# Performance work log

Hardware: AMD Instinct MI355X
Metric: run time of the kernel (lower is better)

## Reference

```python
import jax, jax.numpy as jnp
import numpy as np

V, E, H = 50000, 200, 128
B, R, S, W = 16, 10, 20, 64


def gru_last(x, lengths, Wih, Whh, bih, bhh, reverse=False):
    # x: [N,T,D], lengths: [N] -> final valid hidden state [N,H]
    # Masked-update scan: h only updates on valid timesteps, so after the full
    # scan h equals the packed-sequence final hidden (fwd: t=len-1; bwd: t=0).
    N, T, _ = x.shape
    Hd = Whh.shape[1]
    xi = x @ Wih.T + bih                      # [N,T,3H] input gates, precomputed
    t = jnp.arange(T)
    if reverse:
        xi = xi[:, ::-1]
        valid = (T - 1 - t)[None, :] < lengths[:, None]
    else:
        valid = t[None, :] < lengths[:, None]

    def step(h, inp):
        xg, v = inp
        hg = h @ Whh.T + bhh
        r = jax.nn.sigmoid(xg[:, :Hd] + hg[:, :Hd])
        z = jax.nn.sigmoid(xg[:, Hd:2 * Hd] + hg[:, Hd:2 * Hd])
        n = jnp.tanh(xg[:, 2 * Hd:] + r * hg[:, 2 * Hd:])
        hn = (1.0 - z) * n + z * h
        return jnp.where(v[:, None], hn, h), None

    h0 = jnp.zeros((N, Hd), x.dtype)
    hT, _ = jax.lax.scan(step, h0, (jnp.swapaxes(xi, 0, 1), valid.T))
    return hT


def bigru_last(x, lengths, pf, pb):
    hf = gru_last(x, lengths, *pf, reverse=False)
    hb = gru_last(x, lengths, *pb, reverse=True)
    return 0.5 * (hf + hb)  # reduce bidirectional h_n to hid_dim (mean of dirs)


def setup_inputs() -> dict:
    key = jax.random.key(0)
    ks = jax.random.split(key, 24)

    def gn(k, shape, s=0.1):
        return jax.random.normal(k, shape, dtype=jnp.float32) * s

    return {
        "inputs": jax.random.randint(ks[0], (B, R, S, W), 0, V),
        "sent_lengths": jax.random.randint(ks[1], (B, R, S), 1, W + 1),
        "sent_counts": jax.random.randint(ks[2], (B, R), 1, S + 1),
        "embed": gn(ks[3], (V, E), 1.0),
        "wWih_f": gn(ks[4], (3 * H, E)), "wWhh_f": gn(ks[5], (3 * H, H)),
        "wbih_f": gn(ks[6], (3 * H,)), "wbhh_f": gn(ks[7], (3 * H,)),
        "wWih_b": gn(ks[8], (3 * H, E)), "wWhh_b": gn(ks[9], (3 * H, H)),
        "wbih_b": gn(ks[10], (3 * H,)), "wbhh_b": gn(ks[11], (3 * H,)),
        "sWih_f": gn(ks[12], (3 * H, H)), "sWhh_f": gn(ks[13], (3 * H, H)),
        "sbih_f": gn(ks[14], (3 * H,)), "sbhh_f": gn(ks[15], (3 * H,)),
        "sWih_b": gn(ks[16], (3 * H, H)), "sWhh_b": gn(ks[17], (3 * H, H)),
        "sbih_b": gn(ks[18], (3 * H,)), "sbhh_b": gn(ks[19], (3 * H,)),
        "fc1_w": gn(ks[20], (H // 2, H)), "fc1_b": gn(ks[21], (H // 2,)),
        "fc2_w": gn(ks[22], (1, H // 2)), "fc2_b": gn(ks[23], (1,)),
    }


def reference(inputs, sent_lengths, sent_counts, embed,
              wWih_f, wWhh_f, wbih_f, wbhh_f, wWih_b, wWhh_b, wbih_b, wbhh_b,
              sWih_f, sWhh_f, sbih_f, sbhh_f, sWih_b, sWhh_b, sbih_b, sbhh_b,
              fc1_w, fc1_b, fc2_w, fc2_b):
    b, r, s, w = inputs.shape
    emb = embed[inputs]                                   # [B,R,S,W,E]
    x = emb.reshape(b * r * s, w, -1)
    wlens = sent_lengths.reshape(-1)
    # Word-level BiGRU over all sentences at once (flattened ragged batch)
    sent_rep = bigru_last(x, wlens,
                          (wWih_f, wWhh_f, wbih_f, wbhh_f),
                          (wWih_b, wWhh_b, wbih_b, wbhh_b))  # [B*R*S, H]
    xs = sent_rep.reshape(b * r, s, -1)
    slens = sent_counts.reshape(-1)
    # Sentence-level BiGRU over all reviews at once
    rev = bigru_last(xs, slens,
                     (sWih_f, sWhh_f, sbih_f, sbhh_f),
                     (sWih_b, sWhh_b, sbih_b, sbhh_b)).reshape(b, r, -1)
    h = jax.nn.selu(rev @ fc1_w.T + fc1_b)                # [B,R,H//2]
    r_stars = (h @ fc2_w.T + fc2_b)[..., 0]               # [B,R]
    p_stars = r_stars.mean(-1)                            # [B]
    return p_stars, r_stars
```

## Files before the change

kernel.cpp:

```cpp
#include <hip/hip_runtime.h>
#include <hip/hip_bf16.h>
#include <cstddef>

#define VOCAB 50000
#define EDIM  200
#define HDIM  128
#define BB 16
#define RR 10
#define SS 20
#define WW 64
#define NSENT (BB*RR*SS)
#define NREV  (BB*RR)
#define G3    (3*HDIM)
#define NPROJ (2*G3)

static __device__ __forceinline__ short f2bf(float f) {
    union { float f; unsigned u; } v; v.f = f;
    unsigned r = v.u + 0x7FFFu + ((v.u >> 16) & 1u);
    return (short)(r >> 16);
}
static __device__ __forceinline__ short f2bf_t(float f) {
    union { float f; unsigned u; } v; v.f = f;
    return (short)(v.u >> 16);
}
static __device__ __forceinline__ float bf2f(short s) {
    union { unsigned u; float f; } v;
    v.u = ((unsigned)(unsigned short)s) << 16;
    return v.f;
}
static __device__ __forceinline__ float frcp(float x) {
    return __builtin_amdgcn_rcpf(x);
}
static __device__ __forceinline__ float fsigmoid(float x) {
    return frcp(1.f + __expf(-x));
}
static __device__ __forceinline__ float ftanh(float x) {
    float y = __expf(-2.f * fabsf(x));
    float t = (1.f - y) * frcp(1.f + y);
    return copysignf(t, x);
}

#define GM_LDK 40

template<int KREAL, int KPAD, bool AVG>
__global__ __launch_bounds__(256, 2) void gemm_mfma_bias(
    const float* __restrict__ A0, const float* __restrict__ A1, int M,
    const float* __restrict__ B0, const float* __restrict__ B1,
    const float* __restrict__ bias0, const float* __restrict__ bias1,
    float* __restrict__ C)
{
    using bf16x8 = __attribute__((ext_vector_type(8))) short;
    using f32x4  = __attribute__((ext_vector_type(4))) float;

    const int ct = blockIdx.x;
    const int rt = blockIdx.y;
    const int tid = threadIdx.x;
    const int lane = tid & 63;
    const int wid  = tid >> 6;
    const int rlane = lane & 15;
    const int kgrp  = lane >> 4;

    const int rowBase = rt * 128;
    const int colBase = ct * 128;
    const float* Bsrc = (colBase < G3) ? B0 : B1;
    const int bcol = (colBase < G3) ? colBase : (colBase - G3);

    __shared__ short Ahi[128][GM_LDK], Alo[128][GM_LDK];
    __shared__ short Bhi[128][GM_LDK], Blo[128][GM_LDK];

    const int wrow = (wid >> 1) * 64;
    const int wcol = (wid & 1) * 64;

    f32x4 acc[4][4];
    #pragma unroll
    for (int i = 0; i < 4; ++i)
        #pragma unroll
        for (int j = 0; j < 4; ++j) acc[i][j] = {0.f, 0.f, 0.f, 0.f};

    const int srow = tid >> 1;
    const int skh  = (tid & 1) << 4;

    for (int k0 = 0; k0 < KPAD; k0 += 32) {
        {
            const int grow = rowBase + srow;
            float v[16];
            #pragma unroll
            for (int i = 0; i < 4; ++i) {
                const int k = k0 + skh + i * 4;
                float4 x = {0.f, 0.f, 0.f, 0.f};
                if (grow < M && k + 3 < KREAL) {
                    x = *(const float4*)&A0[(size_t)grow * KREAL + k];
                    if (AVG) {
                        float4 y = *(const float4*)&A1[(size_t)grow * KREAL + k];
                        x.x = 0.5f * (x.x + y.x); x.y = 0.5f * (x.y + y.y);
                        x.z = 0.5f * (x.z + y.z); x.w = 0.5f * (x.w + y.w);
                    }
                }
                v[4*i+0] = x.x; v[4*i+1] = x.y; v[4*i+2] = x.z; v[4*i+3] = x.w;
            }
            bf16x8 h0, h1, l0, l1;
            #pragma unroll
            for (int i = 0; i < 8; ++i) {
                short a = f2bf_t(v[i]);
                h0[i] = a; l0[i] = f2bf(v[i] - bf2f(a));
                short b = f2bf_t(v[i + 8]);
                h1[i] = b; l1[i] = f2bf(v[i + 8] - bf2f(b));
            }
            *(bf16x8*)&Ahi[srow][skh]     = h0;
            *(bf16x8*)&Ahi[srow][skh + 8] = h1;
            *(bf16x8*)&Alo[srow][skh]     = l0;
            *(bf16x8*)&Alo[srow][skh + 8] = l1;
        }
        {
            const int gcol = bcol + srow;
            float v[16];
            #pragma unroll
            for (int i = 0; i < 4; ++i) {
                const int k = k0 + skh + i * 4;
                float4 x = {0.f, 0.f, 0.f, 0.f};
                if (k + 3 < KREAL)
                    x = *(const float4*)&Bsrc[(size_t)gcol * KREAL + k];
                v[4*i+0] = x.x; v[4*i+1] = x.y; v[4*i+2] = x.z; v[4*i+3] = x.w;
            }
            bf16x8 h0, h1, l0, l1;
            #pragma unroll
            for (int i = 0; i < 8; ++i) {
                short a = f2bf_t(v[i]);
                h0[i] = a; l0[i] = f2bf(v[i] - bf2f(a));
                short b = f2bf_t(v[i + 8]);
                h1[i] = b; l1[i] = f2bf(v[i + 8] - bf2f(b));
            }
            *(bf16x8*)&Bhi[srow][skh]     = h0;
            *(bf16x8*)&Bhi[srow][skh + 8] = h1;
            *(bf16x8*)&Blo[srow][skh]     = l0;
            *(bf16x8*)&Blo[srow][skh + 8] = l1;
        }
        __syncthreads();
        bf16x8 ah[4], al[4], bh[4], bl[4];
        #pragma unroll
        for (int mr = 0; mr < 4; ++mr) {
            ah[mr] = *(const bf16x8*)&Ahi[wrow + mr * 16 + rlane][kgrp * 8];
            al[mr] = *(const bf16x8*)&Alo[wrow + mr * 16 + rlane][kgrp * 8];
        }
        #pragma unroll
        for (int nc = 0; nc < 4; ++nc) {
            bh[nc] = *(const bf16x8*)&Bhi[wcol + nc * 16 + rlane][kgrp * 8];
            bl[nc] = *(const bf16x8*)&Blo[wcol + nc * 16 + rlane][kgrp * 8];
        }
        #pragma unroll
        for (int mr = 0; mr < 4; ++mr)
            #pragma unroll
            for (int nc = 0; nc < 4; ++nc) {
                acc[mr][nc] = __builtin_amdgcn_mfma_f32_16x16x32_bf16(
                    ah[mr], bh[nc], acc[mr][nc], 0, 0, 0);
                acc[mr][nc] = __builtin_amdgcn_mfma_f32_16x16x32_bf16(
                    ah[mr], bl[nc], acc[mr][nc], 0, 0, 0);
                acc[mr][nc] = __builtin_amdgcn_mfma_f32_16x16x32_bf16(
                    al[mr], bh[nc], acc[mr][nc], 0, 0, 0);
            }
        __syncthreads();
    }

    const float* bs = (colBase < G3) ? bias0 : bias1;
    #pragma unroll
    for (int nc = 0; nc < 4; ++nc) {
        const int c = wcol + nc * 16 + rlane;
        const float bv = bs[bcol + c];
        #pragma unroll
        for (int mr = 0; mr < 4; ++mr) {
            #pragma unroll
            for (int r = 0; r < 4; ++r) {
                const int grow = rowBase + wrow + mr * 16 + kgrp * 4 + r;
                if (grow < M)
                    C[(size_t)grow * NPROJ + colBase + c] = acc[mr][nc][r] + bv;
            }
        }
    }
}

__global__ __launch_bounds__(256) void sort_all(
    const int* __restrict__ len1, int* __restrict__ order1,
    const int* __restrict__ len2, int* __restrict__ order2)
{
    __shared__ int hist[65];
    const int tid = threadIdx.x;

    for (int i = tid; i < 65; i += 256) hist[i] = 0;
    __syncthreads();
    for (int i = tid; i < NSENT; i += 256) atomicAdd(&hist[len1[i]], 1);
    __syncthreads();
    if (tid == 0) {
        int acc = 0;
        for (int l = 1; l <= WW; ++l) { int c = hist[l]; hist[l] = acc; acc += c; }
    }
    __syncthreads();
    for (int i = tid; i < NSENT; i += 256) {
        int pos = atomicAdd(&hist[len1[i]], 1);
        order1[pos] = i;
    }
    __syncthreads();
    for (int i = tid; i < 65; i += 256) hist[i] = 0;
    __syncthreads();
    for (int i = tid; i < NREV; i += 256) atomicAdd(&hist[len2[i]], 1);
    __syncthreads();
    if (tid == 0) {
        int acc = 0;
        for (int l = 1; l <= SS; ++l) { int c = hist[l]; hist[l] = acc; acc += c; }
    }
    __syncthreads();
    for (int i = tid; i < NREV; i += 256) {
        int pos = atomicAdd(&hist[len2[i]], 1);
        order2[pos] = i;
    }
}

template<bool WORD, int TMAX>
__global__ __launch_bounds__(512, 2) void gru_mfma(
    const float* __restrict__ table,
    const int*   __restrict__ tokens,
    const int*   __restrict__ lengths,
    const int*   __restrict__ order,
    const float* __restrict__ Whh_f, const float* __restrict__ Whh_b,
    const float* __restrict__ bhh_f, const float* __restrict__ bhh_b,
    float* __restrict__ hout_f, float* __restrict__ hout_b,
    int numSeq, int numTiles)
{
    using bf16x8 = __attribute__((ext_vector_type(8))) short;
    using f32x4  = __attribute__((ext_vector_type(4))) float;

    const int dir  = (blockIdx.x >= numTiles) ? 1 : 0;
    const int rawt = dir ? (blockIdx.x - numTiles) : blockIdx.x;
    const int tile = numTiles - 1 - rawt;
    const int base = tile * 16;
    const int tid  = threadIdx.x;
    const int lane = tid & 63;
    const int wid  = tid >> 6;
    const int rlane = lane & 15;
    const int kgrp  = lane >> 4;
    const int e = wid * 16 + rlane;

    __shared__ __align__(16) short sh_hi[2][16][136];
    __shared__ __align__(16) short sh_lo[2][16][136];
    __shared__ int sh_len[16];
    __shared__ int sh_ord[16];
    __shared__ int sh_tok[WORD ? 16 * WW : 1];
    __shared__ int sh_maxlen;

    const float* Whh = dir ? Whh_b : Whh_f;
    const float* bhh = dir ? bhh_b : bhh_f;
    bf16x8 Bhi[3][4], Blo[3][4];
    float bb[3];
    #pragma unroll
    for (int nt = 0; nt < 3; ++nt) {
        const int cb = nt * HDIM + wid * 16;
        const float* wrow = Whh + (size_t)(cb + rlane) * HDIM;
        bb[nt] = bhh[cb + rlane];
        #pragma unroll
        for (int kc = 0; kc < 4; ++kc) {
            const float* wp = wrow + kc * 32 + kgrp * 8;
            float4 w0 = *(const float4*)wp;
            float4 w1 = *(const float4*)(wp + 4);
            float wv[8] = {w0.x, w0.y, w0.z, w0.w, w1.x, w1.y, w1.z, w1.w};
            #pragma unroll
            for (int j = 0; j < 8; ++j) {
                short hi = f2bf_t(wv[j]);
                Bhi[nt][kc][j] = hi;
                Blo[nt][kc][j] = f2bf(wv[j] - bf2f(hi));
            }
        }
    }

    if (tid < 16) {
        int pos = base + tid;
        int seq = (pos < numSeq) ? order[pos] : -1;
        sh_ord[tid] = seq;
        sh_len[tid] = (seq >= 0) ? lengths[seq] : 0;
    }
    __syncthreads();
    if (WORD) {
        for (int f = tid; f < 16 * WW; f += 512) {
            int s = f >> 6;
            int seq = sh_ord[s];
            sh_tok[f] = (seq >= 0) ? tokens[(size_t)seq * WW + (f & 63)] : 0;
        }
    }
    for (int u = tid; u < 2 * 16 * 136; u += 512) {
        ((short*)sh_hi)[u] = 0;
        ((short*)sh_lo)[u] = 0;
    }
    if (tid == 0) {
        int m = 0;
        for (int s = 0; s < 16; ++s) m = max(m, sh_len[s]);
        sh_maxlen = m;
    }
    int lens[4], ords[4];
    #pragma unroll
    for (int j = 0; j < 4; ++j) {
        lens[j] = sh_len[4 * kgrp + j];
        ords[j] = sh_ord[4 * kgrp + j];
    }
    __syncthreads();
    const int maxlen = sh_maxlen;

    auto fetch_xg = [&](int t, float* fr, float* fz, float* fn) {
        #pragma unroll
        for (int j = 0; j < 4; ++j) {
            fr[j] = 0.f; fz[j] = 0.f; fn[j] = 0.f;
            if (t < lens[j]) {
                int tt = dir ? (lens[j] - 1 - t) : t;
                size_t row;
                if (WORD) row = (size_t)sh_tok[(4 * kgrp + j) * WW + tt];
                else      row = (size_t)ords[j] * TMAX + tt;
                const float* xg = table + row * NPROJ + dir * G3 + e;
                fr[j] = xg[0]; fz[j] = xg[HDIM]; fn[j] = xg[2 * HDIM];
            }
        }
    };

    float hold[4] = {0.f, 0.f, 0.f, 0.f};
    float pAr[4], pAz[4], pAn[4];
    float pBr[4], pBz[4], pBn[4];
    fetch_xg(0, pAr, pAz, pAn);
    fetch_xg(1, pBr, pBz, pBn);

#define GRU_STEP(T, PR, PZ, PN)                                               \
    {                                                                         \
        const int cur = (T) & 1, nxt = cur ^ 1;                               \
        bf16x8 ah[4], al[4];                                                  \
        _Pragma("unroll")                                                     \
        for (int kc = 0; kc < 4; ++kc) {                                      \
            ah[kc] = *(const bf16x8*)&sh_hi[cur][rlane][kc * 32 + kgrp * 8];  \
            al[kc] = *(const bf16x8*)&sh_lo[cur][rlane][kc * 32 + kgrp * 8];  \
        }                                                                     \
        f32x4 acc[3];                                                         \
        _Pragma("unroll")                                                     \
        for (int nt = 0; nt < 3; ++nt) {                                      \
            acc[nt] = {0.f, 0.f, 0.f, 0.f};                                   \
            _Pragma("unroll")                                                 \
            for (int kc = 0; kc < 4; ++kc)                                    \
                acc[nt] = __builtin_amdgcn_mfma_f32_16x16x32_bf16(            \
                    ah[kc], Bhi[nt][kc], acc[nt], 0, 0, 0);                   \
            _Pragma("unroll")                                                 \
            for (int kc = 0; kc < 4; ++kc)                                    \
                acc[nt] = __builtin_amdgcn_mfma_f32_16x16x32_bf16(            \
                    ah[kc], Blo[nt][kc], acc[nt], 0, 0, 0);                   \
            _Pragma("unroll")                                                 \
            for (int kc = 0; kc < 4; ++kc)                                    \
                acc[nt] = __builtin_amdgcn_mfma_f32_16x16x32_bf16(            \
                    al[kc], Bhi[nt][kc], acc[nt], 0, 0, 0);                   \
        }                                                                     \
        _Pragma("unroll")                                                     \
        for (int j = 0; j < 4; ++j) {                                         \
            if ((T) < lens[j]) {                                              \
                float hgr = acc[0][j] + bb[0];                                \
                float hgz = acc[1][j] + bb[1];                                \
                float hgn = acc[2][j] + bb[2];                                \
                float rg = fsigmoid(PR[j] + hgr);                             \
                float zg = fsigmoid(PZ[j] + hgz);                             \
                float ng = ftanh(PN[j] + rg * hgn);                           \
                hold[j] = (1.f - zg) * ng + zg * hold[j];                     \
            }                                                                 \
        }                                                                     \
        fetch_xg((T) + 2, PR, PZ, PN);                                        \
        _Pragma("unroll")                                                     \
        for (int j = 0; j < 4; ++j) {                                         \
            const int s = 4 * kgrp + j;                                       \
            short hi = f2bf_t(hold[j]);                                       \
            sh_hi[nxt][s][e] = hi;                                            \
            sh_lo[nxt][s][e] = f2bf(hold[j] - bf2f(hi));                      \
        }                                                                     \
        __syncthreads();                                                      \
    }

    int t = 0;
    for (; t + 1 < maxlen; t += 2) {
        GRU_STEP(t,     pAr, pAz, pAn);
        GRU_STEP(t + 1, pBr, pBz, pBn);
    }
    if (t < maxlen) {
        GRU_STEP(t, pAr, pAz, pAn);
    }
#undef GRU_STEP

    float* hout = dir ? hout_b : hout_f;
    #pragma unroll
    for (int j = 0; j < 4; ++j) {
        if (ords[j] >= 0)
            hout[(size_t)ords[j] * HDIM + e] = hold[j];
    }
}

__global__ __launch_bounds__(64) void head_kernel(
    const float* __restrict__ hsf, const float* __restrict__ hsb,
    const float* __restrict__ fc1_w, const float* __restrict__ fc1_b,
    const float* __restrict__ fc2_w, const float* __restrict__ fc2_b,
    float* __restrict__ out)
{
    const int br = blockIdx.x;
    const int j = threadIdx.x;
    __shared__ float rev[HDIM];
    for (int ee = j; ee < HDIM; ee += 64)
        rev[ee] = 0.5f * (hsf[(size_t)br * HDIM + ee] + hsb[(size_t)br * HDIM + ee]);
    __syncthreads();
    float acc = 0.f;
    #pragma unroll
    for (int k = 0; k < HDIM; ++k)
        acc = fmaf(fc1_w[(size_t)j * HDIM + k], rev[k], acc);
    acc += fc1_b[j];
    const float alpha = 1.6732632423543772f;
    const float scale = 1.0507009873554805f;
    float h1 = scale * (acc > 0.f ? acc : alpha * (expf(acc) - 1.f));
    float contrib = h1 * fc2_w[j];
    #pragma unroll
    for (int off = 32; off > 0; off >>= 1)
        contrib += __shfl_down(contrib, off);
    if (j == 0) out[16 + br] = contrib + fc2_b[0];
}

__global__ void mean_kernel(float* __restrict__ out)
{
    int b = threadIdx.x;
    if (b < BB) {
        float s = 0.f;
        for (int r = 0; r < RR; ++r) s += out[16 + b * RR + r];
        out[b] = s / (float)RR;
    }
}

extern "C" void kernel_launch(void* const* d_in, const int* in_sizes, int n_in,
                              void* d_out, int out_size, void* d_ws, size_t ws_size,
                              hipStream_t stream)
{
    const int*   inputs       = (const int*)d_in[0];
    const int*   sent_lengths = (const int*)d_in[1];
    const int*   sent_counts  = (const int*)d_in[2];
    const float* embed   = (const float*)d_in[3];
    const float* wWih_f  = (const float*)d_in[4];
    const float* wWhh_f  = (const float*)d_in[5];
    const float* wbih_f  = (const float*)d_in[6];
    const float* wbhh_f  = (const float*)d_in[7];
    const float* wWih_b  = (const float*)d_in[8];
    const float* wWhh_b  = (const float*)d_in[9];
    const float* wbih_b  = (const float*)d_in[10];
    const float* wbhh_b  = (const float*)d_in[11];
    const float* sWih_f  = (const float*)d_in[12];
    const float* sWhh_f  = (const float*)d_in[13];
    const float* sbih_f  = (const float*)d_in[14];
    const float* sbhh_f  = (const float*)d_in[15];
    const float* sWih_b  = (const float*)d_in[16];
    const float* sWhh_b  = (const float*)d_in[17];
    const float* sbih_b  = (const float*)d_in[18];
    const float* sbhh_b  = (const float*)d_in[19];
    const float* fc1_w   = (const float*)d_in[20];
    const float* fc1_b   = (const float*)d_in[21];
    const float* fc2_w   = (const float*)d_in[22];
    const float* fc2_b   = (const float*)d_in[23];

    float* ws = (float*)d_ws;
    const size_t projT_elems = (size_t)VOCAB * NPROJ;
    const size_t xgs_elems   = (size_t)NSENT * NPROJ;
    const size_t h_elems     = (size_t)NSENT * HDIM;
    const size_t hs_elems    = (size_t)NREV * HDIM;
    float* projT = ws;
    float* xgs   = projT + projT_elems;
    float* hf    = xgs + xgs_elems;
    float* hb    = hf + h_elems;
    float* hsf   = hb + h_elems;
    float* hsb   = hsf + hs_elems;
    int* order1 = (int*)(hsb + hs_elems);
    int* order2 = order1 + NSENT;

    size_t need = (projT_elems + xgs_elems + 2*h_elems + 2*hs_elems) * sizeof(float)
                + (NSENT + NREV) * sizeof(int);
    if (ws_size < need) return;

    sort_all<<<1, 256, 0, stream>>>(sent_lengths, order1, sent_counts, order2);

    {
        dim3 grid(NPROJ / 128, (VOCAB + 127) / 128);
        gemm_mfma_bias<EDIM, 224, false><<<grid, 256, 0, stream>>>(
            embed, nullptr, VOCAB,
            wWih_f, wWih_b, wbih_f, wbih_b, projT);
    }
    {
        int numTiles = NSENT / 16;
        gru_mfma<true, WW><<<2 * numTiles, 512, 0, stream>>>(
            projT, inputs, sent_lengths, order1,
            wWhh_f, wWhh_b, wbhh_f, wbhh_b,
            hf, hb, NSENT, numTiles);
    }
    {
        dim3 grid(NPROJ / 128, (NSENT + 127) / 128);
        gemm_mfma_bias<HDIM, HDIM, true><<<grid, 256, 0, stream>>>(
            hf, hb, NSENT,
            sWih_f, sWih_b, sbih_f, sbih_b, xgs);
    }
    {
        int numTiles = NREV / 16;
        gru_mfma<false, SS><<<2 * numTiles, 512, 0, stream>>>(
            xgs, nullptr, sent_counts, order2,
            sWhh_f, sWhh_b, sbhh_f, sbhh_b,
            hsf, hsb, NREV, numTiles);
    }
    head_kernel<<<NREV, 64, 0, stream>>>(hsf, hsb, fc1_w, fc1_b, fc2_w, fc2_b,
                                         (float*)d_out);
    mean_kernel<<<1, 64, 0, stream>>>((float*)d_out);
}
```

Baseline: 275.2 us.

## Pre-split operands into bf16 hi/lo buffers before the projection GEMMs

Adds a preconversion kernel that splits the fp32 embedding table, the input weights and the averaged hidden states into padded bf16 hi/lo arrays in workspace. A new GEMM then loads these bf16 tiles directly instead of converting fp32 inside the GEMM loop, and runs with higher occupancy. This removes per-tile split work from the GEMM inner loop, but adds extra kernel launches and a full write plus re-read of the whole embedding table on every call. The new path runs only when the workspace is large enough, otherwise the old GEMM is kept.

```diff
diff --git a/kernel.cpp b/kernel.cpp
--- a/kernel.cpp
+++ b/kernel.cpp
@@ -13,6 +13,7 @@
 #define NREV  (BB*RR)
 #define G3    (3*HDIM)
 #define NPROJ (2*G3)
+#define MPAD_V 50048
 
 static __device__ __forceinline__ short f2bf(float f) {
     union { float f; unsigned u; } v; v.f = f;
@@ -38,6 +39,137 @@
     float y = __expf(-2.f * fabsf(x));
     float t = (1.f - y) * frcp(1.f + y);
     return copysignf(t, x);
+}
+
+using bf16x8 = __attribute__((ext_vector_type(8))) short;
+using f32x4  = __attribute__((ext_vector_type(4))) float;
+
+template<int KREAL, int KPAD, bool AVG>
+__global__ __launch_bounds__(256) void preconv(
+    const float* __restrict__ A0, const float* __restrict__ A1, int Mreal,
+    short* __restrict__ hi, short* __restrict__ lo, int ngroups)
+{
+    int g = blockIdx.x * 256 + threadIdx.x;
+    if (g >= ngroups) return;
+    int row = g / (KPAD / 8);
+    int k   = (g % (KPAD / 8)) * 8;
+    float v[8];
+    if (row < Mreal && k < KREAL) {
+        const float* p = A0 + (size_t)row * KREAL + k;
+        float4 a = *(const float4*)p;
+        float4 b = *(const float4*)(p + 4);
+        if (AVG) {
+            const float* q = A1 + (size_t)row * KREAL + k;
+            float4 c = *(const float4*)q;
+            float4 d = *(const float4*)(q + 4);
+            a.x = 0.5f*(a.x+c.x); a.y = 0.5f*(a.y+c.y);
+            a.z = 0.5f*(a.z+c.z); a.w = 0.5f*(a.w+c.w);
+            b.x = 0.5f*(b.x+d.x); b.y = 0.5f*(b.y+d.y);
+            b.z = 0.5f*(b.z+d.z); b.w = 0.5f*(b.w+d.w);
+        }
+        v[0]=a.x; v[1]=a.y; v[2]=a.z; v[3]=a.w;
+        v[4]=b.x; v[5]=b.y; v[6]=b.z; v[7]=b.w;
+    } else {
+        #pragma unroll
+        for (int j = 0; j < 8; ++j) v[j] = 0.f;
+    }
+    bf16x8 h, l;
+    #pragma unroll
+    for (int j = 0; j < 8; ++j) {
+        short t = f2bf_t(v[j]);
+        h[j] = t;
+        l[j] = f2bf(v[j] - bf2f(t));
+    }
+    *(bf16x8*)&hi[(size_t)row * KPAD + k] = h;
+    *(bf16x8*)&lo[(size_t)row * KPAD + k] = l;
+}
+
+template<int KPAD>
+__global__ __launch_bounds__(256, 4) void gemm_v2(
+    const short* __restrict__ Ahi_g, const short* __restrict__ Alo_g, int M,
+    const short* __restrict__ Bhi_g, const short* __restrict__ Blo_g,
+    const float* __restrict__ bias0, const float* __restrict__ bias1,
+    float* __restrict__ C)
+{
+    const int ct = blockIdx.x;
+    const int rt = blockIdx.y;
+    const int tid = threadIdx.x;
+    const int lane = tid & 63;
+    const int wid  = tid >> 6;
+    const int rlane = lane & 15;
+    const int kgrp  = lane >> 4;
+
+    const int rowBase = rt * 128;
+    const int colBase = ct * 128;
+
+    __shared__ __align__(16) short Ah[128][40], Al[128][40];
+    __shared__ __align__(16) short Bh[128][40], Bl[128][40];
+
+    const int wrow = (wid >> 1) * 64;
+    const int wcol = (wid & 1) * 64;
+
+    f32x4 acc[4][4];
+    #pragma unroll
+    for (int i = 0; i < 4; ++i)
+        #pragma unroll
+        for (int j = 0; j < 4; ++j) acc[i][j] = {0.f, 0.f, 0.f, 0.f};
+
+    const int srow = tid >> 1;
+    const int skh  = (tid & 1) << 4;
+    const size_t arow = (size_t)(rowBase + srow) * KPAD;
+    const size_t brow = (size_t)(colBase + srow) * KPAD;
+
+    for (int k0 = 0; k0 < KPAD; k0 += 32) {
+        *(bf16x8*)&Ah[srow][skh]     = *(const bf16x8*)&Ahi_g[arow + k0 + skh];
+        *(bf16x8*)&Ah[srow][skh + 8] = *(const bf16x8*)&Ahi_g[arow + k0 + skh + 8];
+        *(bf16x8*)&Al[srow][skh]     = *(const bf16x8*)&Alo_g[arow + k0 + skh];
+        *(bf16x8*)&Al[srow][skh + 8] = *(const bf16x8*)&Alo_g[arow + k0 + skh + 8];
+        *(bf16x8*)&Bh[srow][skh]     = *(const bf16x8*)&Bhi_g[brow + k0 + skh];
+        *(bf16x8*)&Bh[srow][skh + 8] = *(const bf16x8*)&Bhi_g[brow + k0 + skh + 8];
+        *(bf16x8*)&Bl[srow][skh]     = *(const bf16x8*)&Blo_g[brow + k0 + skh];
+        *(bf16x8*)&Bl[srow][skh + 8] = *(const bf16x8*)&Blo_g[brow + k0 + skh + 8];
+        __syncthreads();
+        bf16x8 ah[4], al[4], bh[4], bl[4];
+        #pragma unroll
+        for (int mr = 0; mr < 4; ++mr) {
+            ah[mr] = *(const bf16x8*)&Ah[wrow + mr * 16 + rlane][kgrp * 8];
+            al[mr] = *(const bf16x8*)&Al[wrow + mr * 16 + rlane][kgrp * 8];
+        }
+        #pragma unroll
+        for (int nc = 0; nc < 4; ++nc) {
+            bh[nc] = *(const bf16x8*)&Bh[wcol + nc * 16 + rlane][kgrp * 8];
+            bl[nc] = *(const bf16x8*)&Bl[wcol + nc * 16 + rlane][kgrp * 8];
+        }
+        #pragma unroll
+        for (int mr = 0; mr < 4; ++mr)
+            #pragma unroll
+            for (int nc = 0; nc < 4; ++nc) {
+                acc[mr][nc] = __builtin_amdgcn_mfma_f32_16x16x32_bf16(
+                    ah[mr], bh[nc], acc[mr][nc], 0, 0, 0);
+                acc[mr][nc] = __builtin_amdgcn_mfma_f32_16x16x32_bf16(
+                    ah[mr], bl[nc], acc[mr][nc], 0, 0, 0);
+                acc[mr][nc] = __builtin_amdgcn_mfma_f32_16x16x32_bf16(
+                    al[mr], bh[nc], acc[mr][nc], 0, 0, 0);
+            }
+        __syncthreads();
+    }
+
+    const float* bs = (colBase < G3) ? bias0 : bias1;
+    const int bcol = (colBase < G3) ? colBase : (colBase - G3);
+    #pragma unroll
+    for (int nc = 0; nc < 4; ++nc) {
+        const int c = wcol + nc * 16 + rlane;
+        const float bv = bs[bcol + c];
+        #pragma unroll
+        for (int mr = 0; mr < 4; ++mr) {
+            #pragma unroll
+            for (int r = 0; r < 4; ++r) {
+                const int grow = rowBase + wrow + mr * 16 + kgrp * 4 + r;
+                if (grow < M)
+                    C[(size_t)grow * NPROJ + colBase + c] = acc[mr][nc][r] + bv;
+            }
+        }
+    }
 }
 
 #define GM_LDK 40
@@ -49,9 +181,6 @@
     const float* __restrict__ bias0, const float* __restrict__ bias1,
     float* __restrict__ C)
 {
-    using bf16x8 = __attribute__((ext_vector_type(8))) short;
-    using f32x4  = __attribute__((ext_vector_type(4))) float;
-
     const int ct = blockIdx.x;
     const int rt = blockIdx.y;
     const int tid = threadIdx.x;
@@ -225,9 +354,6 @@
     float* __restrict__ hout_f, float* __restrict__ hout_b,
     int numSeq, int numTiles)
 {
-    using bf16x8 = __attribute__((ext_vector_type(8))) short;
-    using f32x4  = __attribute__((ext_vector_type(4))) float;
-
     const int dir  = (blockIdx.x >= numTiles) ? 1 : 0;
     const int rawt = dir ? (blockIdx.x - numTiles) : blockIdx.x;
     const int tile = numTiles - 1 - rawt;
@@ -470,18 +596,54 @@
     int* order1 = (int*)(hsb + hs_elems);
     int* order2 = order1 + NSENT;
 
-    size_t need = (projT_elems + xgs_elems + 2*h_elems + 2*hs_elems) * sizeof(float)
-                + (NSENT + NREV) * sizeof(int);
-    if (ws_size < need) return;
+    const size_t need_base = (projT_elems + xgs_elems + 2*h_elems + 2*hs_elems)
+                             * sizeof(float) + (NSENT + NREV) * sizeof(int);
+    if (ws_size < need_base) return;
+
+    short* Aemb_hi = (short*)(order2 + NREV);
+    short* Aemb_lo = Aemb_hi + (size_t)MPAD_V * 224;
+    short* Bw_hi   = Aemb_lo + (size_t)MPAD_V * 224;
+    short* Bw_lo   = Bw_hi + 768 * 224;
+    short* Sw_hi   = Bw_lo + 768 * 224;
+    short* Sw_lo   = Sw_hi + 768 * 128;
+    short* Ah_hi   = Sw_lo + 768 * 128;
+    short* Ah_lo   = Ah_hi + (size_t)NSENT * HDIM;
+    const size_t blob_shorts = 2 * ((size_t)MPAD_V * 224 + 768 * 224
+                                    + 768 * 128 + (size_t)NSENT * HDIM);
+    const size_t need_v2 = need_base + blob_shorts * sizeof(short);
+    const bool use_v2 = (ws_size >= need_v2);
 
     sort_all<<<1, 256, 0, stream>>>(sent_lengths, order1, sent_counts, order2);
 
-    {
+    if (use_v2) {
+        {
+            int ng = MPAD_V * 224 / 8;
+            preconv<EDIM, 224, false><<<(ng + 255) / 256, 256, 0, stream>>>(
+                embed, nullptr, VOCAB, Aemb_hi, Aemb_lo, ng);
+        }
+        {
+            int ng = 384 * 224 / 8;
+            preconv<EDIM, 224, false><<<(ng + 255) / 256, 256, 0, stream>>>(
+                wWih_f, nullptr, 384, Bw_hi, Bw_lo, ng);
+            preconv<EDIM, 224, false><<<(ng + 255) / 256, 256, 0, stream>>>(
+                wWih_b, nullptr, 384, Bw_hi + 384 * 224, Bw_lo + 384 * 224, ng);
+        }
+        {
+            int ng = 384 * 128 / 8;
+            preconv<HDIM, HDIM, false><<<(ng + 255) / 256, 256, 0, stream>>>(
+                sWih_f, nullptr, 384, Sw_hi, Sw_lo, ng);
+            preconv<HDIM, HDIM, false><<<(ng + 255) / 256, 256, 0, stream>>>(
+                sWih_b, nullptr, 384, Sw_hi + 384 * 128, Sw_lo + 384 * 128, ng);
+        }
+        dim3 grid(NPROJ / 128, MPAD_V / 128);
+        gemm_v2<224><<<grid, 256, 0, stream>>>(
+            Aemb_hi, Aemb_lo, VOCAB, Bw_hi, Bw_lo, wbih_f, wbih_b, projT);
+    } else {
         dim3 grid(NPROJ / 128, (VOCAB + 127) / 128);
         gemm_mfma_bias<EDIM, 224, false><<<grid, 256, 0, stream>>>(
-            embed, nullptr, VOCAB,
-            wWih_f, wWih_b, wbih_f, wbih_b, projT);
-    }
+            embed, nullptr, VOCAB, wWih_f, wWih_b, wbih_f, wbih_b, projT);
+    }
+
     {
         int numTiles = NSENT / 16;
         gru_mfma<true, WW><<<2 * numTiles, 512, 0, stream>>>(
@@ -489,12 +651,20 @@
             wWhh_f, wWhh_b, wbhh_f, wbhh_b,
             hf, hb, NSENT, numTiles);
     }
-    {
+
+    if (use_v2) {
+        int ng = NSENT * HDIM / 8;
+        preconv<HDIM, HDIM, true><<<(ng + 255) / 256, 256, 0, stream>>>(
+            hf, hb, NSENT, Ah_hi, Ah_lo, ng);
+        dim3 grid(NPROJ / 128, NSENT / 128);
+        gemm_v2<128><<<grid, 256, 0, stream>>>(
+            Ah_hi, Ah_lo, NSENT, Sw_hi, Sw_lo, sbih_f, sbih_b, xgs);
+    } else {
         dim3 grid(NPROJ / 128, (NSENT + 127) / 128);
         gemm_mfma_bias<HDIM, HDIM, true><<<grid, 256, 0, stream>>>(
-            hf, hb, NSENT,
-            sWih_f, sWih_b, sbih_f, sbih_b, xgs);
-    }
+            hf, hb, NSENT, sWih_f, sWih_b, sbih_f, sbih_b, xgs);
+    }
+
     {
         int numTiles = NREV / 16;
         gru_mfma<false, SS><<<2 * numTiles, 512, 0, stream>>>(
@@ -502,6 +672,7 @@
             sWhh_f, sWhh_b, sbhh_f, sbhh_b,
             hsf, hsb, NREV, numTiles);
     }
+
     head_kernel<<<NREV, 64, 0, stream>>>(hsf, hsb, fc1_w, fc1_b, fc2_w, fc2_b,
                                          (float*)d_out);
     mean_kernel<<<1, 64, 0, stream>>>((float*)d_out);
```

Result: slower. 284.2 us (+3.3%).

## Merge forward and backward GRU directions into one 1024-thread block per tile

Applied to the files above, without the earlier changes.

Each GRU block now handles both directions for a 16-sequence tile: waves 0-7 run the forward pass and waves 8-15 the backward pass, each using its own shared hidden-state buffers. This halves the grid, and the two directions share the token/length/order loads and the block's maxlen loop. The per-step __syncthreads now spans 16 waves, so every step waits on both directions, and the 1024-thread blocks with launch_bounds(1024,4) put more pressure on registers, which may limit occupancy or cause spills.

```diff
diff --git a/kernel.cpp b/kernel.cpp
--- a/kernel.cpp
+++ b/kernel.cpp
@@ -40,6 +40,9 @@
     return copysignf(t, x);
 }
 
+using bf16x8 = __attribute__((ext_vector_type(8))) short;
+using f32x4  = __attribute__((ext_vector_type(4))) float;
+
 #define GM_LDK 40
 
 template<int KREAL, int KPAD, bool AVG>
@@ -49,9 +52,6 @@
     const float* __restrict__ bias0, const float* __restrict__ bias1,
     float* __restrict__ C)
 {
-    using bf16x8 = __attribute__((ext_vector_type(8))) short;
-    using f32x4  = __attribute__((ext_vector_type(4))) float;
-
     const int ct = blockIdx.x;
     const int rt = blockIdx.y;
     const int tid = threadIdx.x;
@@ -215,7 +215,7 @@
 }
 
 template<bool WORD, int TMAX>
-__global__ __launch_bounds__(512, 2) void gru_mfma(
+__global__ __launch_bounds__(1024, 4) void gru_mfma2(
     const float* __restrict__ table,
     const int*   __restrict__ tokens,
     const int*   __restrict__ lengths,
@@ -225,22 +225,19 @@
     float* __restrict__ hout_f, float* __restrict__ hout_b,
     int numSeq, int numTiles)
 {
-    using bf16x8 = __attribute__((ext_vector_type(8))) short;
-    using f32x4  = __attribute__((ext_vector_type(4))) float;
-
-    const int dir  = (blockIdx.x >= numTiles) ? 1 : 0;
-    const int rawt = dir ? (blockIdx.x - numTiles) : blockIdx.x;
-    const int tile = numTiles - 1 - rawt;
+    const int tile = numTiles - 1 - (int)blockIdx.x;
     const int base = tile * 16;
     const int tid  = threadIdx.x;
     const int lane = tid & 63;
     const int wid  = tid >> 6;
+    const int dir  = wid >> 3;
+    const int w8   = wid & 7;
     const int rlane = lane & 15;
     const int kgrp  = lane >> 4;
-    const int e = wid * 16 + rlane;
-
-    __shared__ __align__(16) short sh_hi[2][16][136];
-    __shared__ __align__(16) short sh_lo[2][16][136];
+    const int e = w8 * 16 + rlane;
+
+    __shared__ __align__(16) short sh_hi[2][2][16][136];
+    __shared__ __align__(16) short sh_lo[2][2][16][136];
     __shared__ int sh_len[16];
     __shared__ int sh_ord[16];
     __shared__ int sh_tok[WORD ? 16 * WW : 1];
@@ -252,7 +249,7 @@
     float bb[3];
     #pragma unroll
     for (int nt = 0; nt < 3; ++nt) {
-        const int cb = nt * HDIM + wid * 16;
+        const int cb = nt * HDIM + w8 * 16;
         const float* wrow = Whh + (size_t)(cb + rlane) * HDIM;
         bb[nt] = bhh[cb + rlane];
         #pragma unroll
@@ -278,13 +275,13 @@
     }
     __syncthreads();
     if (WORD) {
-        for (int f = tid; f < 16 * WW; f += 512) {
+        for (int f = tid; f < 16 * WW; f += 1024) {
             int s = f >> 6;
             int seq = sh_ord[s];
             sh_tok[f] = (seq >= 0) ? tokens[(size_t)seq * WW + (f & 63)] : 0;
         }
     }
-    for (int u = tid; u < 2 * 16 * 136; u += 512) {
+    for (int u = tid; u < 2 * 2 * 16 * 136; u += 1024) {
         ((short*)sh_hi)[u] = 0;
         ((short*)sh_lo)[u] = 0;
     }
@@ -329,8 +326,8 @@
         bf16x8 ah[4], al[4];                                                  \
         _Pragma("unroll")                                                     \
         for (int kc = 0; kc < 4; ++kc) {                                      \
-            ah[kc] = *(const bf16x8*)&sh_hi[cur][rlane][kc * 32 + kgrp * 8];  \
-            al[kc] = *(const bf16x8*)&sh_lo[cur][rlane][kc * 32 + kgrp * 8];  \
+            ah[kc] = *(const bf16x8*)&sh_hi[dir][cur][rlane][kc * 32 + kgrp * 8]; \
+            al[kc] = *(const bf16x8*)&sh_lo[dir][cur][rlane][kc * 32 + kgrp * 8]; \
         }                                                                     \
         f32x4 acc[3];                                                         \
         _Pragma("unroll")                                                     \
@@ -366,8 +363,8 @@
         for (int j = 0; j < 4; ++j) {                                         \
             const int s = 4 * kgrp + j;                                       \
             short hi = f2bf_t(hold[j]);                                       \
-            sh_hi[nxt][s][e] = hi;                                            \
-            sh_lo[nxt][s][e] = f2bf(hold[j] - bf2f(hi));                      \
+            sh_hi[dir][nxt][s][e] = hi;                                       \
+            sh_lo[dir][nxt][s][e] = f2bf(hold[j] - bf2f(hi));                 \
         }                                                                     \
         __syncthreads();                                                      \
     }
@@ -484,7 +481,7 @@
     }
     {
         int numTiles = NSENT / 16;
-        gru_mfma<true, WW><<<2 * numTiles, 512, 0, stream>>>(
+        gru_mfma2<true, WW><<<numTiles, 1024, 0, stream>>>(
             projT, inputs, sent_lengths, order1,
             wWhh_f, wWhh_b, wbhh_f, wbhh_b,
             hf, hb, NSENT, numTiles);
@@ -497,7 +494,7 @@
     }
     {
         int numTiles = NREV / 16;
-        gru_mfma<false, SS><<<2 * numTiles, 512, 0, stream>>>(
+        gru_mfma2<false, SS><<<numTiles, 1024, 0, stream>>>(
             xgs, nullptr, sent_counts, order2,
             sWhh_f, sWhh_b, sbhh_f, sbhh_b,
             hsf, hsb, NREV, numTiles);
```

Result: slower. 836.9 us (+204.1%).

## Pre-convert GEMM weights to split bf16; pair long and short tiles per GRU block

Applied to the files above, without the earlier changes.

Adds a preconv kernel that splits the input-projection weights into hi/lo bf16 once, so the GEMM loads ready bf16 tiles instead of converting fp32 weights in every block. The GRU kernel now processes two 16-sequence tiles per block, pairing a long tile with a short one from opposite ends of the length-sorted order, and interleaves their MFMA work to balance load and add ILP. This halves the GRU grid and doubles its shared memory and register state, which may lower occupancy. It also launches four extra small kernels.

```diff
diff --git a/kernel.cpp b/kernel.cpp
--- a/kernel.cpp
+++ b/kernel.cpp
@@ -40,18 +40,49 @@
     return copysignf(t, x);
 }
 
+using bf16x8 = __attribute__((ext_vector_type(8))) short;
+using f32x4  = __attribute__((ext_vector_type(4))) float;
+
+template<int KREAL, int KPAD>
+__global__ __launch_bounds__(256) void preconv(
+    const float* __restrict__ A0, int Mreal,
+    short* __restrict__ hi, short* __restrict__ lo, int ngroups)
+{
+    int g = blockIdx.x * 256 + threadIdx.x;
+    if (g >= ngroups) return;
+    int row = g / (KPAD / 8);
+    int k   = (g % (KPAD / 8)) * 8;
+    float v[8];
+    if (row < Mreal && k < KREAL) {
+        const float* p = A0 + (size_t)row * KREAL + k;
+        float4 a = *(const float4*)p;
+        float4 b = *(const float4*)(p + 4);
+        v[0]=a.x; v[1]=a.y; v[2]=a.z; v[3]=a.w;
+        v[4]=b.x; v[5]=b.y; v[6]=b.z; v[7]=b.w;
+    } else {
+        #pragma unroll
+        for (int j = 0; j < 8; ++j) v[j] = 0.f;
+    }
+    bf16x8 h, l;
+    #pragma unroll
+    for (int j = 0; j < 8; ++j) {
+        short t = f2bf_t(v[j]);
+        h[j] = t;
+        l[j] = f2bf(v[j] - bf2f(t));
+    }
+    *(bf16x8*)&hi[(size_t)row * KPAD + k] = h;
+    *(bf16x8*)&lo[(size_t)row * KPAD + k] = l;
+}
+
 #define GM_LDK 40
 
 template<int KREAL, int KPAD, bool AVG>
-__global__ __launch_bounds__(256, 2) void gemm_mfma_bias(
+__global__ __launch_bounds__(256, 2) void gemm_v3(
     const float* __restrict__ A0, const float* __restrict__ A1, int M,
-    const float* __restrict__ B0, const float* __restrict__ B1,
+    const short* __restrict__ Bhi_g, const short* __restrict__ Blo_g,
     const float* __restrict__ bias0, const float* __restrict__ bias1,
     float* __restrict__ C)
 {
-    using bf16x8 = __attribute__((ext_vector_type(8))) short;
-    using f32x4  = __attribute__((ext_vector_type(4))) float;
-
     const int ct = blockIdx.x;
     const int rt = blockIdx.y;
     const int tid = threadIdx.x;
@@ -62,8 +93,6 @@
 
     const int rowBase = rt * 128;
     const int colBase = ct * 128;
-    const float* Bsrc = (colBase < G3) ? B0 : B1;
-    const int bcol = (colBase < G3) ? colBase : (colBase - G3);
 
     __shared__ short Ahi[128][GM_LDK], Alo[128][GM_LDK];
     __shared__ short Bhi[128][GM_LDK], Blo[128][GM_LDK];
@@ -79,6 +108,7 @@
 
     const int srow = tid >> 1;
     const int skh  = (tid & 1) << 4;
+    const size_t brow = (size_t)(colBase + srow) * KPAD;
 
     for (int k0 = 0; k0 < KPAD; k0 += 32) {
         {
@@ -111,30 +141,10 @@
             *(bf16x8*)&Alo[srow][skh]     = l0;
             *(bf16x8*)&Alo[srow][skh + 8] = l1;
         }
-        {
-            const int gcol = bcol + srow;
-            float v[16];
-            #pragma unroll
-            for (int i = 0; i < 4; ++i) {
-                const int k = k0 + skh + i * 4;
-                float4 x = {0.f, 0.f, 0.f, 0.f};
-                if (k + 3 < KREAL)
-                    x = *(const float4*)&Bsrc[(size_t)gcol * KREAL + k];
-                v[4*i+0] = x.x; v[4*i+1] = x.y; v[4*i+2] = x.z; v[4*i+3] = x.w;
-            }
-            bf16x8 h0, h1, l0, l1;
-            #pragma unroll
-            for (int i = 0; i < 8; ++i) {
-                short a = f2bf_t(v[i]);
-                h0[i] = a; l0[i] = f2bf(v[i] - bf2f(a));
-                short b = f2bf_t(v[i + 8]);
-                h1[i] = b; l1[i] = f2bf(v[i + 8] - bf2f(b));
-            }
-            *(bf16x8*)&Bhi[srow][skh]     = h0;
-            *(bf16x8*)&Bhi[srow][skh + 8] = h1;
-            *(bf16x8*)&Blo[srow][skh]     = l0;
-            *(bf16x8*)&Blo[srow][skh + 8] = l1;
-        }
+        *(bf16x8*)&Bhi[srow][skh]     = *(const bf16x8*)&Bhi_g[brow + k0 + skh];
+        *(bf16x8*)&Bhi[srow][skh + 8] = *(const bf16x8*)&Bhi_g[brow + k0 + skh + 8];
+        *(bf16x8*)&Blo[srow][skh]     = *(const bf16x8*)&Blo_g[brow + k0 + skh];
+        *(bf16x8*)&Blo[srow][skh + 8] = *(const bf16x8*)&Blo_g[brow + k0 + skh + 8];
         __syncthreads();
         bf16x8 ah[4], al[4], bh[4], bl[4];
         #pragma unroll
@@ -162,6 +172,7 @@
     }
 
     const float* bs = (colBase < G3) ? bias0 : bias1;
+    const int bcol = (colBase < G3) ? colBase : (colBase - G3);
     #pragma unroll
     for (int nc = 0; nc < 4; ++nc) {
         const int c = wcol + nc * 16 + rlane;
@@ -215,7 +226,7 @@
 }
 
 template<bool WORD, int TMAX>
-__global__ __launch_bounds__(512, 2) void gru_mfma(
+__global__ __launch_bounds__(512, 2) void gru_dual(
     const float* __restrict__ table,
     const int*   __restrict__ tokens,
     const int*   __restrict__ lengths,
@@ -225,13 +236,15 @@
     float* __restrict__ hout_f, float* __restrict__ hout_b,
     int numSeq, int numTiles)
 {
-    using bf16x8 = __attribute__((ext_vector_type(8))) short;
-    using f32x4  = __attribute__((ext_vector_type(4))) float;
-
-    const int dir  = (blockIdx.x >= numTiles) ? 1 : 0;
-    const int rawt = dir ? (blockIdx.x - numTiles) : blockIdx.x;
-    const int tile = numTiles - 1 - rawt;
-    const int base = tile * 16;
+    const int halfT = numTiles >> 1;
+    const int b = blockIdx.x;
+    const int dir = (b >= halfT) ? 1 : 0;
+    const int q = dir ? (b - halfT) : b;
+    const int tileA = numTiles - 1 - q;
+    const int tileB = q;
+    const int baseA = tileA * 16;
+    const int baseB = tileB * 16;
+
     const int tid  = threadIdx.x;
     const int lane = tid & 63;
     const int wid  = tid >> 6;
@@ -239,12 +252,12 @@
     const int kgrp  = lane >> 4;
     const int e = wid * 16 + rlane;
 
-    __shared__ __align__(16) short sh_hi[2][16][136];
-    __shared__ __align__(16) short sh_lo[2][16][136];
-    __shared__ int sh_len[16];
-    __shared__ int sh_ord[16];
-    __shared__ int sh_tok[WORD ? 16 * WW : 1];
-    __shared__ int sh_maxlen;
+    __shared__ __align__(16) short shA_hi[2][16][136], shA_lo[2][16][136];
+    __shared__ __align__(16) short shB_hi[2][16][136], shB_lo[2][16][136];
+    __shared__ int shA_len[16], shA_ord[16], shB_len[16], shB_ord[16];
+    __shared__ int shA_tok[WORD ? 16 * WW : 1];
+    __shared__ int shB_tok[WORD ? 16 * WW : 1];
+    __shared__ int sh_ml2[2];
 
     const float* Whh = dir ? Whh_b : Whh_f;
     const float* bhh = dir ? bhh_b : bhh_f;
@@ -271,122 +284,195 @@
     }
 
     if (tid < 16) {
-        int pos = base + tid;
+        int pos = baseA + tid;
         int seq = (pos < numSeq) ? order[pos] : -1;
-        sh_ord[tid] = seq;
-        sh_len[tid] = (seq >= 0) ? lengths[seq] : 0;
+        shA_ord[tid] = seq;
+        shA_len[tid] = (seq >= 0) ? lengths[seq] : 0;
+    } else if (tid < 32) {
+        int u = tid - 16;
+        int pos = baseB + u;
+        int seq = (pos < numSeq) ? order[pos] : -1;
+        shB_ord[u] = seq;
+        shB_len[u] = (seq >= 0) ? lengths[seq] : 0;
     }
     __syncthreads();
     if (WORD) {
         for (int f = tid; f < 16 * WW; f += 512) {
             int s = f >> 6;
-            int seq = sh_ord[s];
-            sh_tok[f] = (seq >= 0) ? tokens[(size_t)seq * WW + (f & 63)] : 0;
+            int sa = shA_ord[s], sb = shB_ord[s];
+            shA_tok[f] = (sa >= 0) ? tokens[(size_t)sa * WW + (f & 63)] : 0;
+            shB_tok[f] = (sb >= 0) ? tokens[(size_t)sb * WW + (f & 63)] : 0;
         }
     }
     for (int u = tid; u < 2 * 16 * 136; u += 512) {
-        ((short*)sh_hi)[u] = 0;
-        ((short*)sh_lo)[u] = 0;
+        ((short*)shA_hi)[u] = 0; ((short*)shA_lo)[u] = 0;
+        ((short*)shB_hi)[u] = 0; ((short*)shB_lo)[u] = 0;
     }
     if (tid == 0) {
         int m = 0;
-        for (int s = 0; s < 16; ++s) m = max(m, sh_len[s]);
-        sh_maxlen = m;
-    }
-    int lens[4], ords[4];
+        for (int s = 0; s < 16; ++s) m = max(m, shA_len[s]);
+        sh_ml2[0] = m;
+    } else if (tid == 1) {
+        int m = 0;
+        for (int s = 0; s < 16; ++s) m = max(m, shB_len[s]);
+        sh_ml2[1] = m;
+    }
+    int lensA[4], ordsA[4], lensB[4], ordsB[4];
     #pragma unroll
     for (int j = 0; j < 4; ++j) {
-        lens[j] = sh_len[4 * kgrp + j];
-        ords[j] = sh_ord[4 * kgrp + j];
-    }
-    __syncthreads();
-    const int maxlen = sh_maxlen;
-
-    auto fetch_xg = [&](int t, float* fr, float* fz, float* fn) {
+        lensA[j] = shA_len[4 * kgrp + j];
+        ordsA[j] = shA_ord[4 * kgrp + j];
+        lensB[j] = shB_len[4 * kgrp + j];
+        ordsB[j] = shB_ord[4 * kgrp + j];
+    }
+    __syncthreads();
+    const int mlA = sh_ml2[0];
+    const int mlB = sh_ml2[1];
+    const int maxt = max(mlA, mlB);
+
+    auto fetchA = [&](int t, float* fr, float* fz, float* fn) {
         #pragma unroll
         for (int j = 0; j < 4; ++j) {
             fr[j] = 0.f; fz[j] = 0.f; fn[j] = 0.f;
-            if (t < lens[j]) {
-                int tt = dir ? (lens[j] - 1 - t) : t;
+            if (t < lensA[j]) {
+                int tt = dir ? (lensA[j] - 1 - t) : t;
                 size_t row;
-                if (WORD) row = (size_t)sh_tok[(4 * kgrp + j) * WW + tt];
-                else      row = (size_t)ords[j] * TMAX + tt;
+                if (WORD) row = (size_t)shA_tok[(4 * kgrp + j) * WW + tt];
+                else      row = (size_t)ordsA[j] * TMAX + tt;
                 const float* xg = table + row * NPROJ + dir * G3 + e;
                 fr[j] = xg[0]; fz[j] = xg[HDIM]; fn[j] = xg[2 * HDIM];
             }
         }
     };
-
-    float hold[4] = {0.f, 0.f, 0.f, 0.f};
+    auto fetchB = [&](int t, float* fr, float* fz, float* fn) {
+        #pragma unroll
+        for (int j = 0; j < 4; ++j) {
+            fr[j] = 0.f; fz[j] = 0.f; fn[j] = 0.f;
+            if (t < lensB[j]) {
+                int tt = dir ? (lensB[j] - 1 - t) : t;
+                size_t row;
+                if (WORD) row = (size_t)shB_tok[(4 * kgrp + j) * WW + tt];
+                else      row = (size_t)ordsB[j] * TMAX + tt;
+                const float* xg = table + row * NPROJ + dir * G3 + e;
+                fr[j] = xg[0]; fz[j] = xg[HDIM]; fn[j] = xg[2 * HDIM];
+            }
+        }
+    };
+
+    float holdA[4] = {0.f, 0.f, 0.f, 0.f};
+    float holdB[4] = {0.f, 0.f, 0.f, 0.f};
     float pAr[4], pAz[4], pAn[4];
     float pBr[4], pBz[4], pBn[4];
-    fetch_xg(0, pAr, pAz, pAn);
-    fetch_xg(1, pBr, pBz, pBn);
-
-#define GRU_STEP(T, PR, PZ, PN)                                               \
-    {                                                                         \
-        const int cur = (T) & 1, nxt = cur ^ 1;                               \
-        bf16x8 ah[4], al[4];                                                  \
-        _Pragma("unroll")                                                     \
-        for (int kc = 0; kc < 4; ++kc) {                                      \
-            ah[kc] = *(const bf16x8*)&sh_hi[cur][rlane][kc * 32 + kgrp * 8];  \
-            al[kc] = *(const bf16x8*)&sh_lo[cur][rlane][kc * 32 + kgrp * 8];  \
-        }                                                                     \
-        f32x4 acc[3];                                                         \
-        _Pragma("unroll")                                                     \
-        for (int nt = 0; nt < 3; ++nt) {                                      \
-            acc[nt] = {0.f, 0.f, 0.f, 0.f};                                   \
-            _Pragma("unroll")                                                 \
-            for (int kc = 0; kc < 4; ++kc)                                    \
-                acc[nt] = __builtin_amdgcn_mfma_f32_16x16x32_bf16(            \
-                    ah[kc], Bhi[nt][kc], acc[nt], 0, 0, 0);                   \
-            _Pragma("unroll")                                                 \
-            for (int kc = 0; kc < 4; ++kc)                                    \
-                acc[nt] = __builtin_amdgcn_mfma_f32_16x16x32_bf16(            \
-                    ah[kc], Blo[nt][kc], acc[nt], 0, 0, 0);                   \
-            _Pragma("unroll")                                                 \
-            for (int kc = 0; kc < 4; ++kc)                                    \
-                acc[nt] = __builtin_amdgcn_mfma_f32_16x16x32_bf16(            \
-                    al[kc], Bhi[nt][kc], acc[nt], 0, 0, 0);                   \
-        }                                                                     \
-        _Pragma("unroll")                                                     \
-        for (int j = 0; j < 4; ++j) {                                         \
-            if ((T) < lens[j]) {                                              \
-                float hgr = acc[0][j] + bb[0];                                \
-                float hgz = acc[1][j] + bb[1];                                \
-                float hgn = acc[2][j] + bb[2];                                \
-                float rg = fsigmoid(PR[j] + hgr);                             \
-                float zg = fsigmoid(PZ[j] + hgz);                             \
-                float ng = ftanh(PN[j] + rg * hgn);                           \
-                hold[j] = (1.f - zg) * ng + zg * hold[j];                     \
-            }                                                                 \
-        }                                                                     \
-        fetch_xg((T) + 2, PR, PZ, PN);                                        \
-        _Pragma("unroll")                                                     \
-        for (int j = 0; j < 4; ++j) {                                         \
-            const int s = 4 * kgrp + j;                                       \
-            short hi = f2bf_t(hold[j]);                                       \
-            sh_hi[nxt][s][e] = hi;                                            \
-            sh_lo[nxt][s][e] = f2bf(hold[j] - bf2f(hi));                      \
-        }                                                                     \
-        __syncthreads();                                                      \
-    }
-
-    int t = 0;
-    for (; t + 1 < maxlen; t += 2) {
-        GRU_STEP(t,     pAr, pAz, pAn);
-        GRU_STEP(t + 1, pBr, pBz, pBn);
-    }
-    if (t < maxlen) {
-        GRU_STEP(t, pAr, pAz, pAn);
-    }
-#undef GRU_STEP
+    fetchA(0, pAr, pAz, pAn);
+    fetchB(0, pBr, pBz, pBn);
+
+    for (int t = 0; t < maxt; ++t) {
+        const int cur = t & 1, nxt = cur ^ 1;
+        const bool actA = (t < mlA), actB = (t < mlB);
+        bf16x8 ahA[4], alA[4], ahB[4], alB[4];
+        f32x4 accA[3], accB[3];
+        if (actA) {
+            #pragma unroll
+            for (int kc = 0; kc < 4; ++kc) {
+                ahA[kc] = *(const bf16x8*)&shA_hi[cur][rlane][kc * 32 + kgrp * 8];
+                alA[kc] = *(const bf16x8*)&shA_lo[cur][rlane][kc * 32 + kgrp * 8];
+            }
+        }
+        if (actB) {
+            #pragma unroll
+            for (int kc = 0; kc < 4; ++kc) {
+                ahB[kc] = *(const bf16x8*)&shB_hi[cur][rlane][kc * 32 + kgrp * 8];
+                alB[kc] = *(const bf16x8*)&shB_lo[cur][rlane][kc * 32 + kgrp * 8];
+            }
+        }
+        if (actA) {
+            #pragma unroll
+            for (int nt = 0; nt < 3; ++nt) {
+                accA[nt] = {0.f, 0.f, 0.f, 0.f};
+                #pragma unroll
+                for (int kc = 0; kc < 4; ++kc)
+                    accA[nt] = __builtin_amdgcn_mfma_f32_16x16x32_bf16(
+                        ahA[kc], Bhi[nt][kc], accA[nt], 0, 0, 0);
+                #pragma unroll
+                for (int kc = 0; kc < 4; ++kc)
+                    accA[nt] = __builtin_amdgcn_mfma_f32_16x16x32_bf16(
+                        ahA[kc], Blo[nt][kc], accA[nt], 0, 0, 0);
+                #pragma unroll
+                for (int kc = 0; kc < 4; ++kc)
+                    accA[nt] = __builtin_amdgcn_mfma_f32_16x16x32_bf16(
+                        alA[kc], Bhi[nt][kc], accA[nt], 0, 0, 0);
+            }
+        }
+        if (actB) {
+            #pragma unroll
+            for (int nt = 0; nt < 3; ++nt) {
+                accB[nt] = {0.f, 0.f, 0.f, 0.f};
+                #pragma unroll
+                for (int kc = 0; kc < 4; ++kc)
+                    accB[nt] = __builtin_amdgcn_mfma_f32_16x16x32_bf16(
+                        ahB[kc], Bhi[nt][kc], accB[nt], 0, 0, 0);
+                #pragma unroll
+                for (int kc = 0; kc < 4; ++kc)
+                    accB[nt] = __builtin_amdgcn_mfma_f32_16x16x32_bf16(
+                        ahB[kc], Blo[nt][kc], accB[nt], 0, 0, 0);
+                #pragma unroll
+                for (int kc = 0; kc < 4; ++kc)
+                    accB[nt] = __builtin_amdgcn_mfma_f32_16x16x32_bf16(
+                        alB[kc], Bhi[nt][kc], accB[nt], 0, 0, 0);
+            }
+        }
+        if (actA) {
+            #pragma unroll
+            for (int j = 0; j < 4; ++j) {
+                if (t < lensA[j]) {
+                    float hgr = accA[0][j] + bb[0];
+                    float hgz = accA[1][j] + bb[1];
+                    float hgn = accA[2][j] + bb[2];
+                    float rg = fsigmoid(pAr[j] + hgr);
+                    float zg = fsigmoid(pAz[j] + hgz);
+                    float ng = ftanh(pAn[j] + rg * hgn);
+                    holdA[j] = (1.f - zg) * ng + zg * holdA[j];
+                }
+            }
+            fetchA(t + 1, pAr, pAz, pAn);
+            #pragma unroll
+            for (int j = 0; j < 4; ++j) {
+                const int s = 4 * kgrp + j;
+                short hi = f2bf_t(holdA[j]);
+                shA_hi[nxt][s][e] = hi;
+                shA_lo[nxt][s][e] = f2bf(holdA[j] - bf2f(hi));
+            }
+        }
+        if (actB) {
+            #pragma unroll
+            for (int j = 0; j < 4; ++j) {
+                if (t < lensB[j]) {
+                    float hgr = accB[0][j] + bb[0];
+                    float hgz = accB[1][j] + bb[1];
+                    float hgn = accB[2][j] + bb[2];
+                    float rg = fsigmoid(pBr[j] + hgr);
+                    float zg = fsigmoid(pBz[j] + hgz);
+                    float ng = ftanh(pBn[j] + rg * hgn);
+                    holdB[j] = (1.f - zg) * ng + zg * holdB[j];
+                }
+            }
+            fetchB(t + 1, pBr, pBz, pBn);
+            #pragma unroll
+            for (int j = 0; j < 4; ++j) {
+                const int s = 4 * kgrp + j;
+                short hi = f2bf_t(holdB[j]);
+                shB_hi[nxt][s][e] = hi;
+                shB_lo[nxt][s][e] = f2bf(holdB[j] - bf2f(hi));
+            }
+        }
+        __syncthreads();
+    }
 
     float* hout = dir ? hout_b : hout_f;
     #pragma unroll
     for (int j = 0; j < 4; ++j) {
-        if (ords[j] >= 0)
-            hout[(size_t)ords[j] * HDIM + e] = hold[j];
+        if (ordsA[j] >= 0) hout[(size_t)ordsA[j] * HDIM + e] = holdA[j];
+        if (ordsB[j] >= 0) hout[(size_t)ordsB[j] * HDIM + e] = holdB[j];
     }
 }
 
@@ -467,37 +553,54 @@
     float* hb    = hf + h_elems;
     float* hsf   = hb + h_elems;
     float* hsb   = hsf + hs_elems;
-    int* order1 = (int*)(hsb + hs_elems);
-    int* order2 = order1 + NSENT;
+    int* order1  = (int*)(hsb + hs_elems);
+    int* order2  = order1 + NSENT;
+    short* Bw_hi = (short*)(order2 + NREV);
+    short* Bw_lo = Bw_hi + 768 * 224;
+    short* Sw_hi = Bw_lo + 768 * 224;
+    short* Sw_lo = Sw_hi + 768 * 128;
 
     size_t need = (projT_elems + xgs_elems + 2*h_elems + 2*hs_elems) * sizeof(float)
-                + (NSENT + NREV) * sizeof(int);
+                + (NSENT + NREV) * sizeof(int)
+                + (size_t)(2 * 768 * 224 + 2 * 768 * 128) * sizeof(short);
     if (ws_size < need) return;
 
     sort_all<<<1, 256, 0, stream>>>(sent_lengths, order1, sent_counts, order2);
+    {
+        int ng = 384 * 224 / 8;
+        preconv<EDIM, 224><<<(ng + 255) / 256, 256, 0, stream>>>(
+            wWih_f, 384, Bw_hi, Bw_lo, ng);
+        preconv<EDIM, 224><<<(ng + 255) / 256, 256, 0, stream>>>(
+            wWih_b, 384, Bw_hi + 384 * 224, Bw_lo + 384 * 224, ng);
+    }
+    {
+        int ng = 384 * 128 / 8;
+        preconv<HDIM, HDIM><<<(ng + 255) / 256, 256, 0, stream>>>(
+            sWih_f, 384, Sw_hi, Sw_lo, ng);
+        preconv<HDIM, HDIM><<<(ng + 255) / 256, 256, 0, stream>>>(
+            sWih_b, 384, Sw_hi + 384 * 128, Sw_lo + 384 * 128, ng);
+    }
 
     {
         dim3 grid(NPROJ / 128, (VOCAB + 127) / 128);
-        gemm_mfma_bias<EDIM, 224, false><<<grid, 256, 0, stream>>>(
-            embed, nullptr, VOCAB,
-            wWih_f, wWih_b, wbih_f, wbih_b, projT);
+        gemm_v3<EDIM, 224, false><<<grid, 256, 0, stream>>>(
+            embed, nullptr, VOCAB, Bw_hi, Bw_lo, wbih_f, wbih_b, projT);
     }
     {
         int numTiles = NSENT / 16;
-        gru_mfma<true, WW><<<2 * numTiles, 512, 0, stream>>>(
+        gru_dual<true, WW><<<numTiles, 512, 0, stream>>>(
             projT, inputs, sent_lengths, order1,
             wWhh_f, wWhh_b, wbhh_f, wbhh_b,
             hf, hb, NSENT, numTiles);
     }
     {
         dim3 grid(NPROJ / 128, (NSENT + 127) / 128);
-        gemm_mfma_bias<HDIM, HDIM, true><<<grid, 256, 0, stream>>>(
-            hf, hb, NSENT,
-            sWih_f, sWih_b, sbih_f, sbih_b, xgs);
+        gemm_v3<HDIM, HDIM, true><<<grid, 256, 0, stream>>>(
+            hf, hb, NSENT, Sw_hi, Sw_lo, sbih_f, sbih_b, xgs);
     }
     {
         int numTiles = NREV / 16;
-        gru_mfma<false, SS><<<2 * numTiles, 512, 0, stream>>>(
+        gru_dual<false, SS><<<numTiles, 512, 0, stream>>>(
             xgs, nullptr, sent_counts, order2,
             sWhh_f, sWhh_b, sbhh_f, sbhh_b,
             hsf, hsb, NREV, numTiles);
```

Measured after the change: 312.6 us. +13.6%, slower.
